# Optimization experiments

Measured on AMD Instinct MI355X. Metric: run time of the kernel, lower is better.

## Reference

```python
import jax, jax.numpy as jnp
import numpy as np

SCALE = 1.0 / (100.0 ** 0.5)  # module hard-codes QK / sqrt(100)


def setup_inputs() -> dict:
    key = jax.random.key(0)
    k1, k2, k3 = jax.random.split(key, 3)
    B, S, D = 8, 2048, 512
    head_size = 64
    x = jax.random.normal(k1, (B, S, D), dtype=jnp.float32)
    kernel = jax.random.normal(k2, (3, D, head_size), dtype=jnp.float32) * 0.02
    dense = jax.random.normal(k3, (D, D), dtype=jnp.float32) * 0.02
    return {"x": x, "kernel": kernel, "dense": dense, "heads": 8}


def reference(x, kernel, dense, heads):
    # All heads use the SAME kernel slices in the original loop, so each
    # iteration produces an identical V; compute once and tile.
    WQ = jnp.einsum('bsd,dh->bsh', x, kernel[0])  # [B,S,Hd]
    WK = jnp.einsum('bsd,dh->bsh', x, kernel[1])
    WV = jnp.einsum('bsd,dh->bsh', x, kernel[2])
    scores = jnp.einsum('bqh,bkh->bqk', WQ, WK) * SCALE  # [B,S,S]
    attn = jax.nn.softmax(scores, axis=-1)
    V = jnp.einsum('bqk,bkh->bqh', attn, WV)  # [B,S,Hd]
    out = jnp.tile(V, (1, 1, heads))  # concat of identical heads -> [B,S,heads*Hd]
    return jnp.einsum('bsf,fo->bso', out, dense)
```

## Files before the change

### kernel.cpp

```cpp
#include <hip/hip_runtime.h>
#include <math.h>


typedef __bf16 bf16;
typedef __bf16 bf16x4v __attribute__((ext_vector_type(4)));
typedef __bf16 bf16x8v __attribute__((ext_vector_type(8)));
typedef float f32x4 __attribute__((ext_vector_type(4)));

namespace {
constexpr int kS = 2048;
constexpr int kD = 512;
constexpr int kRows = 16384;
}

#define MFMA16(a, b, c) __builtin_amdgcn_mfma_f32_16x16x32_bf16((a), (b), (c), 0, 0, 0)

__global__ __launch_bounds__(256) void prep_kernel(const float* __restrict__ w,
                                                   const float* __restrict__ dense,
                                                   bf16* __restrict__ wtg,
                                                   bf16* __restrict__ drt) {
  const int bid = blockIdx.x, tid = threadIdx.x;
  __shared__ float T[64][65];

  if (bid < 24) {
    const int mat = bid >> 3, k0 = (bid & 7) * 64;
#pragma unroll
    for (int p = 0; p < 16; ++p) {
      int e = tid + p * 256;
      int r = e >> 6, n = e & 63;
      T[r][n] = w[mat * 32768 + (k0 + r) * 64 + n];
    }
    __syncthreads();
#pragma unroll
    for (int p = 0; p < 16; ++p) {
      int e = tid + p * 256;
      int n = e >> 6, c = e & 63;
      wtg[(size_t)mat * 32768 + (size_t)n * 512 + k0 + c] = (bf16)T[c][n];
    }
  } else {
    const int o0 = (bid - 24) * 64;
    const int oo = tid & 63, jg = tid >> 6;
    float a[16];
#pragma unroll
    for (int i = 0; i < 16; ++i) a[i] = 0.f;
#pragma unroll
    for (int h = 0; h < 8; ++h)
#pragma unroll
      for (int i = 0; i < 16; ++i)
        a[i] += dense[(size_t)(h * 64 + jg * 16 + i) * kD + o0 + oo];
#pragma unroll
    for (int i = 0; i < 16; ++i) T[oo][jg * 16 + i] = a[i];
    __syncthreads();
#pragma unroll
    for (int p = 0; p < 16; ++p) {
      int e = tid + p * 256;
      int r = e >> 6, j = e & 63;
      drt[(size_t)(o0 + r) * 64 + j] = (bf16)T[r][j];
    }
  }
}

__global__ __launch_bounds__(512) void proj_kernel(const float* __restrict__ x,
                                                   const bf16* __restrict__ wtg,
                                                   bf16* __restrict__ wq,
                                                   bf16* __restrict__ wk,
                                                   bf16* __restrict__ wvt) {
  const int bt = blockIdx.x;
  const int tid = threadIdx.x;
  const int w = tid >> 6, tx = tid & 15, quad = (tid >> 4) & 3;
  const int rt = w & 3, nh = w >> 2;
  const int row0 = bt * 64;

  __shared__ bf16 Xs[64 * 72];
  __shared__ bf16 Wts[3 * 64 * 72];

  f32x4 acc[6];
#pragma unroll
  for (int j = 0; j < 6; ++j) acc[j] = (f32x4){0.f, 0.f, 0.f, 0.f};

  const int xr0 = tid >> 4, xc4 = (tid & 15) * 4;
  const float* xb0 = &x[(size_t)(row0 + xr0) * kD + xc4];
  const float* xb1 = &x[(size_t)(row0 + xr0 + 32) * kD + xc4];
  const int wn = tid >> 3, wc8 = (tid & 7) * 8;
  const bf16* wb = &wtg[(size_t)wn * 512 + wc8];

  float4 xf0, xf1;
  uint4 wf0, wf1, wf2;
#define PROJ_ISSUE(K0)                        \
  do {                                        \
    xf0 = *(const float4*)(xb0 + (K0));       \
    xf1 = *(const float4*)(xb1 + (K0));       \
    wf0 = *(const uint4*)(wb + (K0));         \
    wf1 = *(const uint4*)(wb + 32768 + (K0)); \
    wf2 = *(const uint4*)(wb + 65536 + (K0)); \
  } while (0)

  PROJ_ISSUE(0);
  for (int k0 = 0; k0 < kD; k0 += 64) {
    __syncthreads();
    {
      bf16x4v h0 = {(bf16)xf0.x, (bf16)xf0.y, (bf16)xf0.z, (bf16)xf0.w};
      *(bf16x4v*)&Xs[xr0 * 72 + xc4] = h0;
      bf16x4v h1 = {(bf16)xf1.x, (bf16)xf1.y, (bf16)xf1.z, (bf16)xf1.w};
      *(bf16x4v*)&Xs[(xr0 + 32) * 72 + xc4] = h1;
      *(uint4*)&Wts[(0 * 64 + wn) * 72 + wc8] = wf0;
      *(uint4*)&Wts[(1 * 64 + wn) * 72 + wc8] = wf1;
      *(uint4*)&Wts[(2 * 64 + wn) * 72 + wc8] = wf2;
    }
    if (k0 + 64 < kD) PROJ_ISSUE(k0 + 64);
    __syncthreads();
#pragma unroll
    for (int s = 0; s < 2; ++s) {
      bf16x8v a = *(bf16x8v*)&Xs[(rt * 16 + tx) * 72 + s * 32 + quad * 8];
#pragma unroll
      for (int j = 0; j < 6; ++j) {
        int ntg = nh * 6 + j;
        bf16x8v bfr = *(bf16x8v*)&Wts[(ntg * 16 + tx) * 72 + s * 32 + quad * 8];
        acc[j] = MFMA16(a, bfr, acc[j]);
      }
    }
  }

#pragma unroll
  for (int j = 0; j < 6; ++j) {
    int ntg = nh * 6 + j, mat = ntg >> 2, nt = ntg & 3;
    if (mat < 2) {
      bf16* dst = mat ? wk : wq;
#pragma unroll
      for (int r = 0; r < 4; ++r) {
        int row_g = row0 + rt * 16 + quad * 4 + r;
        dst[(size_t)row_g * 64 + nt * 16 + tx] = (bf16)acc[j][r];
      }
    }
  }
  __syncthreads();
  bf16* Vt = Xs;
#pragma unroll
  for (int j = 0; j < 6; ++j) {
    int ntg = nh * 6 + j, mat = ntg >> 2, nt = ntg & 3;
    if (mat == 2) {
#pragma unroll
      for (int r = 0; r < 4; ++r)
        Vt[(nt * 16 + tx) * 72 + rt * 16 + quad * 4 + r] = (bf16)acc[j][r];
    }
  }
  __syncthreads();
  {
    int v = tid >> 3, seg = tid & 7;
    *(uint4*)&wvt[(size_t)v * kRows + row0 + seg * 8] =
        *(uint4*)&Vt[v * 72 + seg * 8];
  }
}

__global__ __launch_bounds__(512, 2) void flash_kernel(
    const bf16* __restrict__ wq, const bf16* __restrict__ wk,
    const bf16* __restrict__ wvt, const bf16* __restrict__ drt,
    float* __restrict__ out) {
  const int bid = blockIdx.x;
  const int b = bid & 7, qb = bid >> 3;
  const int q0 = qb * 32;
  const int tid = threadIdx.x;
  const int w = tid >> 6, lane = tid & 63, tx = tid & 15, quad = (tid >> 4) & 3;

  __shared__ __align__(16) char lds[65536];
  __shared__ float Lsh[256];
  __shared__ __align__(16) bf16 vob[32 * 64];
  bf16* Ksw = (bf16*)(lds + w * 8192);
  bf16* Psw = (bf16*)(lds + w * 8192 + 4096);

  const bf16* wqb = wq + (size_t)(b * kS) * 64;
  const bf16* wkb = wk + (size_t)(b * kS) * 64;
  const bf16* wvb = wvt + b * kS;

  const int kc0 = (quad ^ (tx & 7)) * 8;
  const int kc1 = ((4 + quad) ^ (tx & 7)) * 8;
  const int h2 = (tx ^ (tx >> 2)) & 3;

  bf16x8v aq[2][2];
#pragma unroll
  for (int rt = 0; rt < 2; ++rt)
#pragma unroll
    for (int s = 0; s < 2; ++s)
      aq[rt][s] = *(const bf16x8v*)&wqb[(size_t)(q0 + rt * 16 + tx) * 64 +
                                        s * 32 + quad * 8];

  f32x4 oacc[2][4];
#pragma unroll
  for (int rt = 0; rt < 2; ++rt)
#pragma unroll
    for (int nt = 0; nt < 4; ++nt) oacc[rt][nt] = (f32x4){0.f, 0.f, 0.f, 0.f};
  float lsum[2][4] = {};

  const int ksr = lane >> 3, kslc = lane & 7;
  const int koff = (kslc ^ ksr) * 8;

  const bf16* kap = &wkb[(size_t)ksr * 64 + kslc * 8];
  const bf16* vfp = &wvb[(size_t)tx * kRows + quad * 8];

  uint4 kr0, kr1, kr2, kr3;
#define KR_ISSUE(TT)                                \
  do {                                              \
    const size_t kb = (size_t)(((TT)*8 + w) * 32);  \
    kr0 = *(const uint4*)(kap + kb * 64);           \
    kr1 = *(const uint4*)(kap + kb * 64 + 8 * 64);  \
    kr2 = *(const uint4*)(kap + kb * 64 + 16 * 64); \
    kr3 = *(const uint4*)(kap + kb * 64 + 24 * 64); \
  } while (0)

  KR_ISSUE(0);
  for (int t = 0; t < 8; ++t) {
    const int k0 = (t * 8 + w) * 32;

    bf16x8v vb0 = *(const bf16x8v*)(vfp + (size_t)0 * 16 * kRows + k0);
    bf16x8v vb1 = *(const bf16x8v*)(vfp + (size_t)1 * 16 * kRows + k0);
    bf16x8v vb2 = *(const bf16x8v*)(vfp + (size_t)2 * 16 * kRows + k0);
    bf16x8v vb3 = *(const bf16x8v*)(vfp + (size_t)3 * 16 * kRows + k0);

    *(uint4*)&Ksw[(ksr + 0) * 64 + koff] = kr0;
    *(uint4*)&Ksw[(ksr + 8) * 64 + koff] = kr1;
    *(uint4*)&Ksw[(ksr + 16) * 64 + koff] = kr2;
    *(uint4*)&Ksw[(ksr + 24) * 64 + koff] = kr3;
    if (t < 7) KR_ISSUE(t + 1);

#pragma unroll
    for (int nt = 0; nt < 2; ++nt) {
      int krow = nt * 16 + tx;
      bf16x8v b0 = *(bf16x8v*)&Ksw[krow * 64 + kc0];
      bf16x8v b1 = *(bf16x8v*)&Ksw[krow * 64 + kc1];
#pragma unroll
      for (int rt = 0; rt < 2; ++rt) {
        f32x4 z = (f32x4){0.f, 0.f, 0.f, 0.f};
        z = MFMA16(aq[rt][0], b0, z);
        z = MFMA16(aq[rt][1], b1, z);
#pragma unroll
        for (int r = 0; r < 4; ++r) {
          float p = __expf(z[r] * 0.1f);
          lsum[rt][r] += p;
          int q = rt * 16 + quad * 4 + r;
          int chunk = nt * 2 + (tx >> 3);
          Psw[q * 32 + ((chunk ^ (r ^ quad)) * 8) + (tx & 7)] = (bf16)p;
        }
      }
    }

#pragma unroll
    for (int rt = 0; rt < 2; ++rt) {
      bf16x8v pa = *(bf16x8v*)&Psw[(rt * 16 + tx) * 32 + ((quad ^ h2) * 8)];
      oacc[rt][0] = MFMA16(pa, vb0, oacc[rt][0]);
      oacc[rt][1] = MFMA16(pa, vb1, oacc[rt][1]);
      oacc[rt][2] = MFMA16(pa, vb2, oacc[rt][2]);
      oacc[rt][3] = MFMA16(pa, vb3, oacc[rt][3]);
    }
  }

  __syncthreads();
  float* myO = (float*)(lds + w * 8192);
  float* myL = Lsh + w * 32;
#pragma unroll
  for (int rt = 0; rt < 2; ++rt)
#pragma unroll
    for (int nt = 0; nt < 4; ++nt)
#pragma unroll
      for (int r = 0; r < 4; ++r)
        myO[(rt * 16 + quad * 4 + r) * 64 + nt * 16 + tx] = oacc[rt][nt][r];
#pragma unroll
  for (int rt = 0; rt < 2; ++rt)
#pragma unroll
    for (int r = 0; r < 4; ++r) {
      float v = lsum[rt][r];
#pragma unroll
      for (int m = 1; m < 16; m <<= 1) v += __shfl_xor(v, m, 64);
      if (tx == 0) myL[rt * 16 + quad * 4 + r] = v;
    }
  __syncthreads();

#pragma unroll
  for (int p = 0; p < 4; ++p) {
    int e = tid + p * 512;
    int row = e >> 6, col = e & 63;
    float s = 0.f, lt = 0.f;
#pragma unroll
    for (int wv = 0; wv < 8; ++wv) {
      s += ((const float*)(lds + wv * 8192))[e];
      lt += Lsh[wv * 32 + row];
    }
    vob[row * 64 + (((col >> 3) ^ (row & 7)) * 8) + (col & 7)] = (bf16)(s / lt);
  }
  __syncthreads();

  bf16x8v av[2][2];
#pragma unroll
  for (int rt = 0; rt < 2; ++rt) {
    av[rt][0] = *(bf16x8v*)&vob[(rt * 16 + tx) * 64 + kc0];
    av[rt][1] = *(bf16x8v*)&vob[(rt * 16 + tx) * 64 + kc1];
  }

  float* OutS = (float*)lds;
#pragma unroll
  for (int c = 0; c < 2; ++c) {
    if (c) __syncthreads();
#pragma unroll
    for (int i = 0; i < 2; ++i) {
      const int ct = c * 16 + w * 2 + i;
      bf16x8v bd0 =
          *(const bf16x8v*)&drt[(size_t)(ct * 16 + tx) * 64 + quad * 8];
      bf16x8v bd1 =
          *(const bf16x8v*)&drt[(size_t)(ct * 16 + tx) * 64 + 32 + quad * 8];
#pragma unroll
      for (int rt = 0; rt < 2; ++rt) {
        f32x4 z = (f32x4){0.f, 0.f, 0.f, 0.f};
        z = MFMA16(av[rt][0], bd0, z);
        z = MFMA16(av[rt][1], bd1, z);
#pragma unroll
        for (int r = 0; r < 4; ++r)
          OutS[(rt * 16 + quad * 4 + r) * 260 + (w * 2 + i) * 16 + tx] = z[r];
      }
    }
    __syncthreads();
#pragma unroll
    for (int p = 0; p < 4; ++p) {
      int e = tid + p * 512;
      int row = e >> 6, seg = e & 63;
      *(float4*)&out[(size_t)(b * kS + q0 + row) * kD + c * 256 + seg * 4] =
          *(float4*)&OutS[row * 260 + seg * 4];
    }
  }
}

extern "C" void kernel_launch(void* const* d_in, const int* in_sizes, int n_in,
                              void* d_out, int out_size, void* d_ws,
                              size_t ws_size, hipStream_t stream) {
  const float* x = (const float*)d_in[0];
  const float* w = (const float*)d_in[1];
  const float* dense = (const float*)d_in[2];
  float* out = (float*)d_out;

  bf16* wq = (bf16*)d_ws;
  bf16* wk = wq + (size_t)kRows * 64;
  bf16* wvt = wk + (size_t)kRows * 64;
  bf16* wtg = wvt + (size_t)kRows * 64;
  bf16* drt = wtg + 98304;

  prep_kernel<<<32, 256, 0, stream>>>(w, dense, wtg, drt);
  proj_kernel<<<256, 512, 0, stream>>>(x, wtg, wq, wk, wvt);
  flash_kernel<<<512, 512, 0, stream>>>(wq, wk, wvt, drt, out);
}
```

Measured before the change: 132.0 us.

## Restructure projection kernel into 16-row blocks loading operands directly from global

```diff
diff --git a/kernel.cpp b/kernel.cpp
--- a/kernel.cpp
+++ b/kernel.cpp
@@ -60,95 +60,59 @@
   }
 }
 
-__global__ __launch_bounds__(512) void proj_kernel(const float* __restrict__ x,
-                                                   const bf16* __restrict__ wtg,
-                                                   bf16* __restrict__ wq,
-                                                   bf16* __restrict__ wk,
-                                                   bf16* __restrict__ wvt) {
-  const int bt = blockIdx.x;
+__global__ __launch_bounds__(256, 4) void proj_kernel(const float* __restrict__ x,
+                                                      const bf16* __restrict__ wtg,
+                                                      bf16* __restrict__ wq,
+                                                      bf16* __restrict__ wk,
+                                                      bf16* __restrict__ wvt) {
+  const int bid = blockIdx.x;
   const int tid = threadIdx.x;
   const int w = tid >> 6, tx = tid & 15, quad = (tid >> 4) & 3;
-  const int rt = w & 3, nh = w >> 2;
-  const int row0 = bt * 64;
-
-  __shared__ bf16 Xs[64 * 72];
-  __shared__ bf16 Wts[3 * 64 * 72];
-
-  f32x4 acc[6];
-#pragma unroll
-  for (int j = 0; j < 6; ++j) acc[j] = (f32x4){0.f, 0.f, 0.f, 0.f};
-
-  const int xr0 = tid >> 4, xc4 = (tid & 15) * 4;
-  const float* xb0 = &x[(size_t)(row0 + xr0) * kD + xc4];
-  const float* xb1 = &x[(size_t)(row0 + xr0 + 32) * kD + xc4];
-  const int wn = tid >> 3, wc8 = (tid & 7) * 8;
-  const bf16* wb = &wtg[(size_t)wn * 512 + wc8];
-
-  float4 xf0, xf1;
-  uint4 wf0, wf1, wf2;
-#define PROJ_ISSUE(K0)                        \
-  do {                                        \
-    xf0 = *(const float4*)(xb0 + (K0));       \
-    xf1 = *(const float4*)(xb1 + (K0));       \
-    wf0 = *(const uint4*)(wb + (K0));         \
-    wf1 = *(const uint4*)(wb + 32768 + (K0)); \
-    wf2 = *(const uint4*)(wb + 65536 + (K0)); \
-  } while (0)
-
-  PROJ_ISSUE(0);
-  for (int k0 = 0; k0 < kD; k0 += 64) {
-    __syncthreads();
-    {
-      bf16x4v h0 = {(bf16)xf0.x, (bf16)xf0.y, (bf16)xf0.z, (bf16)xf0.w};
-      *(bf16x4v*)&Xs[xr0 * 72 + xc4] = h0;
-      bf16x4v h1 = {(bf16)xf1.x, (bf16)xf1.y, (bf16)xf1.z, (bf16)xf1.w};
-      *(bf16x4v*)&Xs[(xr0 + 32) * 72 + xc4] = h1;
-      *(uint4*)&Wts[(0 * 64 + wn) * 72 + wc8] = wf0;
-      *(uint4*)&Wts[(1 * 64 + wn) * 72 + wc8] = wf1;
-      *(uint4*)&Wts[(2 * 64 + wn) * 72 + wc8] = wf2;
-    }
-    if (k0 + 64 < kD) PROJ_ISSUE(k0 + 64);
-    __syncthreads();
-#pragma unroll
-    for (int s = 0; s < 2; ++s) {
-      bf16x8v a = *(bf16x8v*)&Xs[(rt * 16 + tx) * 72 + s * 32 + quad * 8];
-#pragma unroll
-      for (int j = 0; j < 6; ++j) {
-        int ntg = nh * 6 + j;
-        bf16x8v bfr = *(bf16x8v*)&Wts[(ntg * 16 + tx) * 72 + s * 32 + quad * 8];
-        acc[j] = MFMA16(a, bfr, acc[j]);
-      }
-    }
-  }
-
-#pragma unroll
-  for (int j = 0; j < 6; ++j) {
-    int ntg = nh * 6 + j, mat = ntg >> 2, nt = ntg & 3;
+  const int row0 = bid * 16;
+
+  __shared__ bf16 Vt[64 * 24];
+
+  f32x4 acc[3];
+#pragma unroll
+  for (int j = 0; j < 3; ++j) acc[j] = (f32x4){0.f, 0.f, 0.f, 0.f};
+
+  const float* xa = &x[(size_t)(row0 + tx) * kD + quad * 8];
+  const bf16* wbase = &wtg[(size_t)(w * 48 + tx) * 512 + quad * 8];
+
+#pragma unroll 4
+  for (int ks = 0; ks < 16; ++ks) {
+    const int k0 = ks * 32;
+    float4 f0 = *(const float4*)(xa + k0);
+    float4 f1 = *(const float4*)(xa + k0 + 4);
+    bf16x8v a = {(bf16)f0.x, (bf16)f0.y, (bf16)f0.z, (bf16)f0.w,
+                 (bf16)f1.x, (bf16)f1.y, (bf16)f1.z, (bf16)f1.w};
+    bf16x8v b0 = *(const bf16x8v*)(wbase + k0);
+    bf16x8v b1 = *(const bf16x8v*)(wbase + 16 * 512 + k0);
+    bf16x8v b2 = *(const bf16x8v*)(wbase + 32 * 512 + k0);
+    acc[0] = MFMA16(a, b0, acc[0]);
+    acc[1] = MFMA16(a, b1, acc[1]);
+    acc[2] = MFMA16(a, b2, acc[2]);
+  }
+
+#pragma unroll
+  for (int j = 0; j < 3; ++j) {
+    int ntg = w * 3 + j, mat = ntg >> 2, nt = ntg & 3;
     if (mat < 2) {
       bf16* dst = mat ? wk : wq;
 #pragma unroll
-      for (int r = 0; r < 4; ++r) {
-        int row_g = row0 + rt * 16 + quad * 4 + r;
-        dst[(size_t)row_g * 64 + nt * 16 + tx] = (bf16)acc[j][r];
-      }
+      for (int r = 0; r < 4; ++r)
+        dst[(size_t)(row0 + quad * 4 + r) * 64 + nt * 16 + tx] = (bf16)acc[j][r];
+    } else {
+#pragma unroll
+      for (int r = 0; r < 4; ++r)
+        Vt[(nt * 16 + tx) * 24 + quad * 4 + r] = (bf16)acc[j][r];
     }
   }
   __syncthreads();
-  bf16* Vt = Xs;
-#pragma unroll
-  for (int j = 0; j < 6; ++j) {
-    int ntg = nh * 6 + j, mat = ntg >> 2, nt = ntg & 3;
-    if (mat == 2) {
-#pragma unroll
-      for (int r = 0; r < 4; ++r)
-        Vt[(nt * 16 + tx) * 72 + rt * 16 + quad * 4 + r] = (bf16)acc[j][r];
-    }
-  }
-  __syncthreads();
-  {
-    int v = tid >> 3, seg = tid & 7;
+  if (tid < 128) {
+    int v = tid >> 1, seg = tid & 1;
     *(uint4*)&wvt[(size_t)v * kRows + row0 + seg * 8] =
-        *(uint4*)&Vt[v * 72 + seg * 8];
+        *(uint4*)&Vt[v * 24 + seg * 8];
   }
 }
 
@@ -342,6 +306,6 @@
   bf16* drt = wtg + 98304;
 
   prep_kernel<<<32, 256, 0, stream>>>(w, dense, wtg, drt);
-  proj_kernel<<<256, 512, 0, stream>>>(x, wtg, wq, wk, wvt);
+  proj_kernel<<<1024, 256, 0, stream>>>(x, wtg, wq, wk, wvt);
   flash_kernel<<<512, 512, 0, stream>>>(wq, wk, wvt, drt, out);
 }
```

After: 155.6 us. 1.18x slower.

## Software-pipeline flash loop with double-buffered P tile in LDS

Applied to the files above, without the earlier changes.

```diff
diff --git a/kernel.cpp b/kernel.cpp
--- a/kernel.cpp
+++ b/kernel.cpp
@@ -166,7 +166,8 @@
   __shared__ float Lsh[256];
   __shared__ __align__(16) bf16 vob[32 * 64];
   bf16* Ksw = (bf16*)(lds + w * 8192);
-  bf16* Psw = (bf16*)(lds + w * 8192 + 4096);
+  bf16* Ps0 = (bf16*)(lds + w * 8192 + 4096);
+  bf16* Ps1 = (bf16*)(lds + w * 8192 + 6144);
 
   const bf16* wqb = wq + (size_t)(b * kS) * 64;
   const bf16* wkb = wk + (size_t)(b * kS) * 64;
@@ -198,6 +199,7 @@
   const bf16* vfp = &wvb[(size_t)tx * kRows + quad * 8];
 
   uint4 kr0, kr1, kr2, kr3;
+  bf16x8v vb0, vb1, vb2, vb3;
 #define KR_ISSUE(TT)                                \
   do {                                              \
     const size_t kb = (size_t)(((TT)*8 + w) * 32);  \
@@ -207,51 +209,74 @@
     kr3 = *(const uint4*)(kap + kb * 64 + 24 * 64); \
   } while (0)
 
+#define K_DRAIN()                                \
+  do {                                           \
+    *(uint4*)&Ksw[(ksr + 0) * 64 + koff] = kr0;  \
+    *(uint4*)&Ksw[(ksr + 8) * 64 + koff] = kr1;  \
+    *(uint4*)&Ksw[(ksr + 16) * 64 + koff] = kr2; \
+    *(uint4*)&Ksw[(ksr + 24) * 64 + koff] = kr3; \
+  } while (0)
+
+#define QK_SM(PW)                                                          \
+  do {                                                                     \
+    _Pragma("unroll") for (int nt = 0; nt < 2; ++nt) {                     \
+      int krow = nt * 16 + tx;                                             \
+      bf16x8v b0 = *(bf16x8v*)&Ksw[krow * 64 + kc0];                       \
+      bf16x8v b1 = *(bf16x8v*)&Ksw[krow * 64 + kc1];                       \
+      _Pragma("unroll") for (int rt = 0; rt < 2; ++rt) {                   \
+        f32x4 z = (f32x4){0.f, 0.f, 0.f, 0.f};                             \
+        z = MFMA16(aq[rt][0], b0, z);                                      \
+        z = MFMA16(aq[rt][1], b1, z);                                      \
+        _Pragma("unroll") for (int r = 0; r < 4; ++r) {                    \
+          float p = __expf(z[r] * 0.1f);                                   \
+          lsum[rt][r] += p;                                                \
+          int q = rt * 16 + quad * 4 + r;                                  \
+          int chunk = nt * 2 + (tx >> 3);                                  \
+          (PW)[q * 32 + ((chunk ^ (r ^ quad)) * 8) + (tx & 7)] = (bf16)p;  \
+        }                                                                  \
+      }                                                                    \
+    }                                                                      \
+  } while (0)
+
+#define PV(PR)                                                             \
+  do {                                                                     \
+    _Pragma("unroll") for (int rt = 0; rt < 2; ++rt) {                     \
+      bf16x8v pa = *(bf16x8v*)&(PR)[(rt * 16 + tx) * 32 + ((quad ^ h2) * 8)]; \
+      oacc[rt][0] = MFMA16(pa, vb0, oacc[rt][0]);                          \
+      oacc[rt][1] = MFMA16(pa, vb1, oacc[rt][1]);                          \
+      oacc[rt][2] = MFMA16(pa, vb2, oacc[rt][2]);                          \
+      oacc[rt][3] = MFMA16(pa, vb3, oacc[rt][3]);                          \
+    }                                                                      \
+  } while (0)
+
+#define VB_LOAD(K0)                                                  \
+  do {                                                               \
+    vb0 = *(const bf16x8v*)(vfp + (size_t)0 * 16 * kRows + (K0));    \
+    vb1 = *(const bf16x8v*)(vfp + (size_t)1 * 16 * kRows + (K0));    \
+    vb2 = *(const bf16x8v*)(vfp + (size_t)2 * 16 * kRows + (K0));    \
+    vb3 = *(const bf16x8v*)(vfp + (size_t)3 * 16 * kRows + (K0));    \
+  } while (0)
+
   KR_ISSUE(0);
-  for (int t = 0; t < 8; ++t) {
+  {
+    const int k0 = (0 * 8 + w) * 32;
+    K_DRAIN();
+    KR_ISSUE(1);
+    QK_SM(Ps0);
+    VB_LOAD(k0);
+  }
+#pragma unroll
+  for (int t = 1; t < 8; ++t) {
     const int k0 = (t * 8 + w) * 32;
-
-    bf16x8v vb0 = *(const bf16x8v*)(vfp + (size_t)0 * 16 * kRows + k0);
-    bf16x8v vb1 = *(const bf16x8v*)(vfp + (size_t)1 * 16 * kRows + k0);
-    bf16x8v vb2 = *(const bf16x8v*)(vfp + (size_t)2 * 16 * kRows + k0);
-    bf16x8v vb3 = *(const bf16x8v*)(vfp + (size_t)3 * 16 * kRows + k0);
-
-    *(uint4*)&Ksw[(ksr + 0) * 64 + koff] = kr0;
-    *(uint4*)&Ksw[(ksr + 8) * 64 + koff] = kr1;
-    *(uint4*)&Ksw[(ksr + 16) * 64 + koff] = kr2;
-    *(uint4*)&Ksw[(ksr + 24) * 64 + koff] = kr3;
+    bf16* pw = (t & 1) ? Ps1 : Ps0;
+    bf16* pr = (t & 1) ? Ps0 : Ps1;
+    K_DRAIN();
     if (t < 7) KR_ISSUE(t + 1);
-
-#pragma unroll
-    for (int nt = 0; nt < 2; ++nt) {
-      int krow = nt * 16 + tx;
-      bf16x8v b0 = *(bf16x8v*)&Ksw[krow * 64 + kc0];
-      bf16x8v b1 = *(bf16x8v*)&Ksw[krow * 64 + kc1];
-#pragma unroll
-      for (int rt = 0; rt < 2; ++rt) {
-        f32x4 z = (f32x4){0.f, 0.f, 0.f, 0.f};
-        z = MFMA16(aq[rt][0], b0, z);
-        z = MFMA16(aq[rt][1], b1, z);
-#pragma unroll
-        for (int r = 0; r < 4; ++r) {
-          float p = __expf(z[r] * 0.1f);
-          lsum[rt][r] += p;
-          int q = rt * 16 + quad * 4 + r;
-          int chunk = nt * 2 + (tx >> 3);
-          Psw[q * 32 + ((chunk ^ (r ^ quad)) * 8) + (tx & 7)] = (bf16)p;
-        }
-      }
-    }
-
-#pragma unroll
-    for (int rt = 0; rt < 2; ++rt) {
-      bf16x8v pa = *(bf16x8v*)&Psw[(rt * 16 + tx) * 32 + ((quad ^ h2) * 8)];
-      oacc[rt][0] = MFMA16(pa, vb0, oacc[rt][0]);
-      oacc[rt][1] = MFMA16(pa, vb1, oacc[rt][1]);
-      oacc[rt][2] = MFMA16(pa, vb2, oacc[rt][2]);
-      oacc[rt][3] = MFMA16(pa, vb3, oacc[rt][3]);
-    }
-  }
+    PV(pr);
+    QK_SM(pw);
+    VB_LOAD(k0);
+  }
+  PV(Ps1);
 
   __syncthreads();
   float* myO = (float*)(lds + w * 8192);
```

Result: no change. 132.2 us (+0.1%).
